# Optimization experiments

Hardware: AMD Instinct MI355X
Metric: run time of the kernel (lower is better)

The kernel has to match this reference:

```python
import jax, jax.numpy as jnp
import numpy as np

T, G = 8, 128                      # time frames, spatial grid per axis
RMIN, RMAX = -1.5, 1.5             # same range for x, y, z
STEP = (RMAX - RMIN) / G           # voxel step per axis
# corner order: [C000, C100, C010, C110, C001, C101, C011, C111]
_OFFSETS = jnp.array([[0,0,0],[1,0,0],[0,1,0],[1,1,0],
                      [0,0,1],[1,0,1],[0,1,1],[1,1,1]], dtype=jnp.int32)

def _trilinear_coef(p):
    # p: [N,3] fractional position inside the cell, in [0,1)
    u, v, w = p[:, 0], p[:, 1], p[:, 2]
    return jnp.stack([(1-u)*(1-v)*(1-w), u*(1-v)*(1-w), (1-u)*v*(1-w), u*v*(1-w),
                      (1-u)*(1-v)*w,     u*(1-v)*w,     (1-u)*v*w,     u*v*w], axis=1)

def setup_inputs() -> dict:
    key = jax.random.key(0)
    k1, k2, k3, k4 = jax.random.split(key, 4)
    N = 1048576
    pos = jax.random.uniform(k1, (N, 3), jnp.float32, RMIN, RMAX)
    t = jax.random.randint(k2, (N,), 0, T, dtype=jnp.int32)
    sigma = jax.random.uniform(k3, (N,), jnp.float32)
    target_norm = jax.random.normal(k4, (N, 3), jnp.float32)
    lr = jnp.full((1,), 0.1, jnp.float32)
    voxel_array = jnp.full((T, G, G, G, 3), jnp.sqrt(1.0 / 3.0), jnp.float32)
    return {"t": t, "pos": pos, "lr": lr, "sigma": sigma,
            "target_norm": target_norm, "voxel_array": voxel_array}

def reference(t, pos, lr, sigma, target_norm, voxel_array):
    # shift into [0, range) coords (all axes share the same range/step)
    pos_s = pos - RMIN
    min_idx = jnp.floor(pos_s / STEP).astype(jnp.int32)          # [N,3], == // in source
    idx = jnp.clip(min_idx[:, None, :] + _OFFSETS[None], 0, G - 1)  # [N,8,3]
    frac = jnp.mod(pos_s, STEP) / STEP                           # [N,3]
    coef = _trilinear_coef(frac)                                 # [N,8]
    xi, yi, zi = idx[..., 0], idx[..., 1], idx[..., 2]
    ti = jnp.broadcast_to(t[:, None], xi.shape)                  # [N,8]
    vertex_values = voxel_array[ti, xi, yi, zi]                  # [N,8,3] gather
    value = jnp.sum(coef[:, :, None] * vertex_values, axis=1)    # [N,3]
    # update weights
    sigma_weight = (1.0 - jnp.exp(-sigma))[:, None]              # [N,1]
    update_lambda = jax.nn.sigmoid(lr * sigma_weight * coef)[..., None]  # [N,8,1]
    new_vertex_values = update_lambda * target_norm[:, None, :] + (1.0 - update_lambda) * vertex_values
    diff = new_vertex_values - vertex_values                     # [N,8,3]
    new_voxel = voxel_array.at[ti.reshape(-1), xi.reshape(-1),
                               yi.reshape(-1), zi.reshape(-1)].add(diff.reshape(-1, 3))
    return value, new_voxel
```

## Files before the change

kernel.cpp:

```cpp
#include <hip/hip_runtime.h>
#include <hip/hip_fp16.h>
#include <math.h>


#define GRES 128
#define NBINS (8 * 128 * 128)
#define SCAN_BLOCKS 512
constexpr float RMIN_F = -1.5f;
constexpr float STEP_F = 3.0f / 128.0f;

__global__ __launch_bounds__(256) void key_hist_kernel(
    const int* __restrict__ t, const float* __restrict__ pos,
    unsigned* __restrict__ keys, unsigned* __restrict__ hist, int N)
{
    int i = blockIdx.x * blockDim.x + threadIdx.x;
    if (i >= N) return;
    float px = pos[3 * i + 0] - RMIN_F;
    float py = pos[3 * i + 1] - RMIN_F;
    int cx = min((int)floorf(px / STEP_F), GRES - 1);
    int cy = min((int)floorf(py / STEP_F), GRES - 1);
    unsigned key  = ((unsigned)t[i] << 14) | ((unsigned)cx << 7) | (unsigned)cy;
    unsigned rank = atomicAdd(&hist[key], 1u);
    keys[i] = (key << 15) | rank;
}

__global__ __launch_bounds__(256) void scanA_kernel(
    const unsigned* __restrict__ hist, unsigned* __restrict__ binstart,
    unsigned* __restrict__ partial)
{
    __shared__ unsigned sh[256];
    const int tid = threadIdx.x;
    const int gid = blockIdx.x * 256 + tid;
    unsigned x = hist[gid];
    sh[tid] = x;
    __syncthreads();
    for (int off = 1; off < 256; off <<= 1) {
        unsigned v = (tid >= off) ? sh[tid - off] : 0u;
        __syncthreads();
        sh[tid] += v;
        __syncthreads();
    }
    binstart[gid] = sh[tid] - x;
    if (tid == 255) partial[blockIdx.x] = sh[255];
}

__global__ __launch_bounds__(512) void scanB_kernel(
    const unsigned* __restrict__ partial, unsigned* __restrict__ offs)
{
    __shared__ unsigned sh[512];
    const int tid = threadIdx.x;
    unsigned x = partial[tid];
    sh[tid] = x;
    __syncthreads();
    for (int off = 1; off < 512; off <<= 1) {
        unsigned v = (tid >= off) ? sh[tid - off] : 0u;
        __syncthreads();
        sh[tid] += v;
        __syncthreads();
    }
    offs[tid] = sh[tid] - x;
}

__global__ __launch_bounds__(256) void scanC_kernel(
    unsigned* __restrict__ binstart, const unsigned* __restrict__ offs, int N)
{
    const int gid = blockIdx.x * 256 + threadIdx.x;
    binstart[gid] += offs[blockIdx.x];
    if (gid == 0) binstart[NBINS] = (unsigned)N;
}

__global__ __launch_bounds__(256) void scatter_kernel(
    const float* __restrict__ pos, const float* __restrict__ lr_p,
    const float* __restrict__ sigma, const float* __restrict__ target,
    const unsigned* __restrict__ keys, const unsigned* __restrict__ binstart,
    uint4* __restrict__ sorted, int N)
{
    int i = blockIdx.x * blockDim.x + threadIdx.x;
    if (i >= N) return;
    unsigned kr   = keys[i];
    unsigned key  = kr >> 15;
    unsigned rank = kr & 0x7fffu;
    unsigned slot = binstart[key] + rank;

    float px = pos[3 * i + 0] - RMIN_F;
    float py = pos[3 * i + 1] - RMIN_F;
    float pz = pos[3 * i + 2] - RMIN_F;
    float u = fmodf(px, STEP_F) / STEP_F;
    float v = fmodf(py, STEP_F) / STEP_F;
    float w = fmodf(pz, STEP_F) / STEP_F;
    int   mz = min((int)floorf(pz / STEP_F), GRES - 1);

    unsigned qu = (unsigned)(u * 2047.0f + 0.5f);
    unsigned qv = (unsigned)(v * 2047.0f + 0.5f);
    unsigned qw = (unsigned)(w * 1023.0f + 0.5f);

    float lrsw = lr_p[0] * (1.0f - expf(-sigma[i]));

    unsigned hx = (unsigned)__half_as_ushort(__float2half(target[3 * i + 0]));
    unsigned hy = (unsigned)__half_as_ushort(__float2half(target[3 * i + 1]));
    unsigned hz = (unsigned)__half_as_ushort(__float2half(target[3 * i + 2]));
    unsigned hl = (unsigned)__half_as_ushort(__float2half(lrsw));

    uint4 p;
    p.x = (qu << 21) | (qv << 10) | qw;
    p.y = ((unsigned)i << 7) | (unsigned)mz;
    p.z = hx | (hy << 16);
    p.w = hz | (hl << 16);
    sorted[slot] = p;
}

__global__ __launch_bounds__(256) void brick_kernel(
    const unsigned* __restrict__ binstart,
    const uint4*    __restrict__ sorted,
    const float*    __restrict__ voxel_in,
    float*          __restrict__ out_value,
    float*          __restrict__ out_voxel)
{
    __shared__ __align__(16) float s_acc[4 * 4 * 128 * 3];
    __shared__ unsigned s_start[25];
    __shared__ unsigned s_pref[26];

    const int vb = ((blockIdx.x & 7) << 10) | (blockIdx.x >> 3);
    const int t  = vb >> 10;
    const int bx = (vb >> 5) & 31;
    const int by = vb & 31;
    const int x0 = bx << 2, y0 = by << 2;
    const int tid = threadIdx.x;
    const size_t tbase = (size_t)t * (GRES * GRES * GRES * 3);

    float4* s_acc4 = (float4*)s_acc;
    for (int q = tid; q < 16 * 96; q += 256) s_acc4[q] = make_float4(0.f, 0.f, 0.f, 0.f);

    if (tid < 25) {
        int dxb = tid / 5 - 1, dyb = tid % 5 - 1;
        int cx = x0 + dxb, cy = y0 + dyb;
        unsigned st = 0, cnt = 0;
        if (cx >= 0 && cx < GRES && cy >= 0 && cy < GRES) {
            unsigned key = ((unsigned)t << 14) | ((unsigned)cx << 7) | (unsigned)cy;
            st  = binstart[key];
            cnt = binstart[key + 1] - st;
        }
        s_start[tid] = st;
        s_pref[tid + 1] = cnt;
    }
    __syncthreads();
    if (tid == 0) {
        unsigned run = 0;
        s_pref[0] = 0;
        for (int b = 0; b < 25; ++b) {
            unsigned c = s_pref[b + 1];
            s_pref[b + 1] = run + c;
            run += c;
        }
    }
    __syncthreads();
    const int P = (int)s_pref[25];

    for (int j = tid; j < P; j += 256) {
        int b = 0;
        while (s_pref[b + 1] <= (unsigned)j) ++b;
        const int dxb = b / 5 - 1, dyb = b % 5 - 1;
        const int cx = x0 + dxb, cy = y0 + dyb;
        const unsigned g = s_start[b] + ((unsigned)j - s_pref[b]);

        const uint4 p = sorted[g];
        const float u = (float)(p.x >> 21)           * (1.0f / 2047.0f);
        const float v = (float)((p.x >> 10) & 2047u) * (1.0f / 2047.0f);
        const float w = (float)(p.x & 1023u)         * (1.0f / 1023.0f);
        const int  mz  = (int)(p.y & 127u);
        const int  idx = (int)(p.y >> 7);
        const float tx = __half2float(__ushort_as_half((unsigned short)(p.z & 0xffffu)));
        const float ty = __half2float(__ushort_as_half((unsigned short)(p.z >> 16)));
        const float tz = __half2float(__ushort_as_half((unsigned short)(p.w & 0xffffu)));
        const float lrsw = __half2float(__ushort_as_half((unsigned short)(p.w >> 16)));

        const int xs1 = min(cx + 1, GRES - 1);
        const int ys1 = min(cy + 1, GRES - 1);
        const int zs1 = min(mz + 1, GRES - 1);

        float a[8][3];
        #pragma unroll
        for (int k = 0; k < 8; ++k) {
            const int xi = (k & 1) ? xs1 : cx;
            const int yi = (k & 2) ? ys1 : cy;
            const int zi = (k & 4) ? zs1 : mz;
            const float* vp = voxel_in + tbase + (((size_t)xi * GRES + yi) * GRES + zi) * 3;
            a[k][0] = vp[0];
            a[k][1] = vp[1];
            a[k][2] = vp[2];
        }

        float c[8];
        c[0] = (1.f - u) * (1.f - v) * (1.f - w);
        c[1] =        u  * (1.f - v) * (1.f - w);
        c[2] = (1.f - u) *        v  * (1.f - w);
        c[3] =        u  *        v  * (1.f - w);
        c[4] = (1.f - u) * (1.f - v) *        w;
        c[5] =        u  * (1.f - v) *        w;
        c[6] = (1.f - u) *        v  *        w;
        c[7] =        u  *        v  *        w;

        const bool owner = (dxb >= 0) && (dyb >= 0);

        float vx = 0.f, vy = 0.f, vz = 0.f;
        #pragma unroll
        for (int k = 0; k < 8; ++k) {
            if (owner) {
                vx += c[k] * a[k][0];
                vy += c[k] * a[k][1];
                vz += c[k] * a[k][2];
            }
            const int xi = (k & 1) ? xs1 : cx;
            const int yi = (k & 2) ? ys1 : cy;
            const int sxi = xi - x0, syi = yi - y0;
            if (sxi >= 0 && sxi < 4 && syi >= 0 && syi < 4) {
                const int zi = (k & 4) ? zs1 : mz;
                const float lam = 1.0f / (1.0f + expf(-lrsw * c[k]));
                const int sa = ((sxi * 4 + syi) * 128 + zi) * 3;
                atomicAdd(&s_acc[sa + 0], lam * (tx - a[k][0]));
                atomicAdd(&s_acc[sa + 1], lam * (ty - a[k][1]));
                atomicAdd(&s_acc[sa + 2], lam * (tz - a[k][2]));
            }
        }
        if (owner) {
            out_value[3 * idx + 0] = vx;
            out_value[3 * idx + 1] = vy;
            out_value[3 * idx + 2] = vz;
        }
    }
    __syncthreads();

    for (int q = tid; q < 16 * 96; q += 256) {
        int row = q / 96, r = q - row * 96;
        int ox = row >> 2, oy = row & 3;
        const size_t coff = tbase + (size_t)(x0 + ox) * 49152 + (size_t)(y0 + oy) * 384;
        float4 a = *((const float4*)(voxel_in + coff) + r);
        float4 d = s_acc4[q];
        *((float4*)(out_voxel + coff) + r) =
            make_float4(a.x + d.x, a.y + d.y, a.z + d.z, a.w + d.w);
    }
}

extern "C" void kernel_launch(void* const* d_in, const int* in_sizes, int n_in,
                              void* d_out, int out_size, void* d_ws, size_t ws_size,
                              hipStream_t stream) {
    const int*   t      = (const int*)  d_in[0];
    const float* pos    = (const float*)d_in[1];
    const float* lr     = (const float*)d_in[2];
    const float* sigma  = (const float*)d_in[3];
    const float* target = (const float*)d_in[4];
    const float* voxel  = (const float*)d_in[5];

    const int N = in_sizes[0];

    float* out_value = (float*)d_out;
    float* out_voxel = out_value + (size_t)3 * N;

    uint4*    sorted   = (uint4*)d_ws;
    unsigned* keys     = (unsigned*)(sorted + (size_t)N);
    unsigned* hist     = keys + N;
    unsigned* binstart = hist + NBINS;
    unsigned* partial  = binstart + (NBINS + 1);
    unsigned* offs     = partial + SCAN_BLOCKS;

    const int block = 256;
    const int grid  = (N + block - 1) / block;

    hipMemsetAsync(hist, 0, NBINS * sizeof(unsigned), stream);
    key_hist_kernel<<<grid, block, 0, stream>>>(t, pos, keys, hist, N);
    scanA_kernel<<<SCAN_BLOCKS, 256, 0, stream>>>(hist, binstart, partial);
    scanB_kernel<<<1, 512, 0, stream>>>(partial, offs);
    scanC_kernel<<<SCAN_BLOCKS, 256, 0, stream>>>(binstart, offs, N);
    scatter_kernel<<<grid, block, 0, stream>>>(pos, lr, sigma, target, keys,
                                               binstart, sorted, N);
    brick_kernel<<<8192, 256, 0, stream>>>(binstart, sorted, voxel,
                                           out_value, out_voxel);
}
```

Measured before the change: 523.7 us.

## Accumulate lambda-weighted sums in shared memory, gather corners only for owners, merge scan

The brick kernel now accumulates sum(lam), sum(lam*target) per voxel in float4 shared slots. The old value is applied once at write-out, so per-particle corner gathers of the voxel array are needed only for owner particles that produce the interpolated value. This rests on the update being linear in the old voxel value. The scanB kernel is removed, and each scanC block reduces its preceding partials itself. The change also uses fast __expf and binary search for the bin lookup. Shared memory grows (float4 per voxel, 4 atomics instead of 3), and the final write-out loses float4 vectorisation in exchange for fewer global gathers.

```diff
diff --git a/kernel.cpp b/kernel.cpp
--- a/kernel.cpp
+++ b/kernel.cpp
@@ -44,28 +44,19 @@
     if (tid == 255) partial[blockIdx.x] = sh[255];
 }
 
-__global__ __launch_bounds__(512) void scanB_kernel(
-    const unsigned* __restrict__ partial, unsigned* __restrict__ offs)
-{
-    __shared__ unsigned sh[512];
-    const int tid = threadIdx.x;
-    unsigned x = partial[tid];
-    sh[tid] = x;
-    __syncthreads();
-    for (int off = 1; off < 512; off <<= 1) {
-        unsigned v = (tid >= off) ? sh[tid - off] : 0u;
-        __syncthreads();
-        sh[tid] += v;
-        __syncthreads();
-    }
-    offs[tid] = sh[tid] - x;
-}
-
 __global__ __launch_bounds__(256) void scanC_kernel(
-    unsigned* __restrict__ binstart, const unsigned* __restrict__ offs, int N)
-{
+    unsigned* __restrict__ binstart, const unsigned* __restrict__ partial, int N)
+{
+    __shared__ unsigned s_w[4];
+    unsigned loc = 0;
+    for (int i = threadIdx.x; i < blockIdx.x; i += 256) loc += partial[i];
+    #pragma unroll
+    for (int off = 32; off > 0; off >>= 1) loc += __shfl_down(loc, off);
+    if ((threadIdx.x & 63) == 0) s_w[threadIdx.x >> 6] = loc;
+    __syncthreads();
+    const unsigned off0 = s_w[0] + s_w[1] + s_w[2] + s_w[3];
     const int gid = blockIdx.x * 256 + threadIdx.x;
-    binstart[gid] += offs[blockIdx.x];
+    binstart[gid] += off0;
     if (gid == 0) binstart[NBINS] = (unsigned)N;
 }
 
@@ -94,7 +85,7 @@
     unsigned qv = (unsigned)(v * 2047.0f + 0.5f);
     unsigned qw = (unsigned)(w * 1023.0f + 0.5f);
 
-    float lrsw = lr_p[0] * (1.0f - expf(-sigma[i]));
+    float lrsw = lr_p[0] * (1.0f - __expf(-sigma[i]));
 
     unsigned hx = (unsigned)__half_as_ushort(__float2half(target[3 * i + 0]));
     unsigned hy = (unsigned)__half_as_ushort(__float2half(target[3 * i + 1]));
@@ -116,7 +107,7 @@
     float*          __restrict__ out_value,
     float*          __restrict__ out_voxel)
 {
-    __shared__ __align__(16) float s_acc[4 * 4 * 128 * 3];
+    __shared__ __align__(16) float4 s_acc[4 * 4 * 128];
     __shared__ unsigned s_start[25];
     __shared__ unsigned s_pref[26];
 
@@ -128,8 +119,7 @@
     const int tid = threadIdx.x;
     const size_t tbase = (size_t)t * (GRES * GRES * GRES * 3);
 
-    float4* s_acc4 = (float4*)s_acc;
-    for (int q = tid; q < 16 * 96; q += 256) s_acc4[q] = make_float4(0.f, 0.f, 0.f, 0.f);
+    for (int q = tid; q < 2048; q += 256) s_acc[q] = make_float4(0.f, 0.f, 0.f, 0.f);
 
     if (tid < 25) {
         int dxb = tid / 5 - 1, dyb = tid % 5 - 1;
@@ -148,9 +138,8 @@
         unsigned run = 0;
         s_pref[0] = 0;
         for (int b = 0; b < 25; ++b) {
-            unsigned c = s_pref[b + 1];
-            s_pref[b + 1] = run + c;
-            run += c;
+            run += s_pref[b + 1];
+            s_pref[b + 1] = run;
         }
     }
     __syncthreads();
@@ -158,7 +147,11 @@
 
     for (int j = tid; j < P; j += 256) {
         int b = 0;
-        while (s_pref[b + 1] <= (unsigned)j) ++b;
+        #pragma unroll
+        for (int s = 16; s > 0; s >>= 1) {
+            int nb = b + s;
+            if (nb <= 24 && s_pref[nb] <= (unsigned)j) b = nb;
+        }
         const int dxb = b / 5 - 1, dyb = b % 5 - 1;
         const int cx = x0 + dxb, cy = y0 + dyb;
         const unsigned g = s_start[b] + ((unsigned)j - s_pref[b]);
@@ -178,18 +171,6 @@
         const int ys1 = min(cy + 1, GRES - 1);
         const int zs1 = min(mz + 1, GRES - 1);
 
-        float a[8][3];
-        #pragma unroll
-        for (int k = 0; k < 8; ++k) {
-            const int xi = (k & 1) ? xs1 : cx;
-            const int yi = (k & 2) ? ys1 : cy;
-            const int zi = (k & 4) ? zs1 : mz;
-            const float* vp = voxel_in + tbase + (((size_t)xi * GRES + yi) * GRES + zi) * 3;
-            a[k][0] = vp[0];
-            a[k][1] = vp[1];
-            a[k][2] = vp[2];
-        }
-
         float c[8];
         c[0] = (1.f - u) * (1.f - v) * (1.f - w);
         c[1] =        u  * (1.f - v) * (1.f - w);
@@ -202,42 +183,61 @@
 
         const bool owner = (dxb >= 0) && (dyb >= 0);
 
-        float vx = 0.f, vy = 0.f, vz = 0.f;
-        #pragma unroll
-        for (int k = 0; k < 8; ++k) {
-            if (owner) {
+        if (owner) {
+            float a[8][3];
+            #pragma unroll
+            for (int k = 0; k < 8; ++k) {
+                const int xi = (k & 1) ? xs1 : cx;
+                const int yi = (k & 2) ? ys1 : cy;
+                const int zi = (k & 4) ? zs1 : mz;
+                const float* vp = voxel_in + tbase + (((size_t)xi * GRES + yi) * GRES + zi) * 3;
+                a[k][0] = vp[0];
+                a[k][1] = vp[1];
+                a[k][2] = vp[2];
+            }
+            float vx = 0.f, vy = 0.f, vz = 0.f;
+            #pragma unroll
+            for (int k = 0; k < 8; ++k) {
                 vx += c[k] * a[k][0];
                 vy += c[k] * a[k][1];
                 vz += c[k] * a[k][2];
             }
+            out_value[3 * idx + 0] = vx;
+            out_value[3 * idx + 1] = vy;
+            out_value[3 * idx + 2] = vz;
+        }
+
+        #pragma unroll
+        for (int k = 0; k < 8; ++k) {
             const int xi = (k & 1) ? xs1 : cx;
             const int yi = (k & 2) ? ys1 : cy;
             const int sxi = xi - x0, syi = yi - y0;
             if (sxi >= 0 && sxi < 4 && syi >= 0 && syi < 4) {
                 const int zi = (k & 4) ? zs1 : mz;
-                const float lam = 1.0f / (1.0f + expf(-lrsw * c[k]));
-                const int sa = ((sxi * 4 + syi) * 128 + zi) * 3;
-                atomicAdd(&s_acc[sa + 0], lam * (tx - a[k][0]));
-                atomicAdd(&s_acc[sa + 1], lam * (ty - a[k][1]));
-                atomicAdd(&s_acc[sa + 2], lam * (tz - a[k][2]));
+                const float lam = 1.0f / (1.0f + __expf(-lrsw * c[k]));
+                float* sa = (float*)&s_acc[(sxi * 4 + syi) * 128 + zi];
+                atomicAdd(sa + 0, lam);
+                atomicAdd(sa + 1, lam * tx);
+                atomicAdd(sa + 2, lam * ty);
+                atomicAdd(sa + 3, lam * tz);
             }
         }
-        if (owner) {
-            out_value[3 * idx + 0] = vx;
-            out_value[3 * idx + 1] = vy;
-            out_value[3 * idx + 2] = vz;
-        }
-    }
-    __syncthreads();
-
-    for (int q = tid; q < 16 * 96; q += 256) {
-        int row = q / 96, r = q - row * 96;
-        int ox = row >> 2, oy = row & 3;
-        const size_t coff = tbase + (size_t)(x0 + ox) * 49152 + (size_t)(y0 + oy) * 384;
-        float4 a = *((const float4*)(voxel_in + coff) + r);
-        float4 d = s_acc4[q];
-        *((float4*)(out_voxel + coff) + r) =
-            make_float4(a.x + d.x, a.y + d.y, a.z + d.z, a.w + d.w);
+    }
+    __syncthreads();
+
+    for (int q = tid; q < 2048; q += 256) {
+        const int col = q >> 7;
+        const int zi  = q & 127;
+        const int ox = col >> 2, oy = col & 3;
+        const size_t coff = tbase + (size_t)(x0 + ox) * 49152
+                                  + (size_t)(y0 + oy) * 384 + 3 * (size_t)zi;
+        const float4 s = s_acc[q];
+        const float ax = voxel_in[coff + 0];
+        const float ay = voxel_in[coff + 1];
+        const float az = voxel_in[coff + 2];
+        out_voxel[coff + 0] = ax + s.y - s.x * ax;
+        out_voxel[coff + 1] = ay + s.z - s.x * ay;
+        out_voxel[coff + 2] = az + s.w - s.x * az;
     }
 }
 
@@ -261,7 +261,6 @@
     unsigned* hist     = keys + N;
     unsigned* binstart = hist + NBINS;
     unsigned* partial  = binstart + (NBINS + 1);
-    unsigned* offs     = partial + SCAN_BLOCKS;
 
     const int block = 256;
     const int grid  = (N + block - 1) / block;
@@ -269,8 +268,7 @@
     hipMemsetAsync(hist, 0, NBINS * sizeof(unsigned), stream);
     key_hist_kernel<<<grid, block, 0, stream>>>(t, pos, keys, hist, N);
     scanA_kernel<<<SCAN_BLOCKS, 256, 0, stream>>>(hist, binstart, partial);
-    scanB_kernel<<<1, 512, 0, stream>>>(partial, offs);
-    scanC_kernel<<<SCAN_BLOCKS, 256, 0, stream>>>(binstart, offs, N);
+    scanC_kernel<<<SCAN_BLOCKS, 256, 0, stream>>>(binstart, partial, N);
     scatter_kernel<<<grid, block, 0, stream>>>(pos, lr, sigma, target, keys,
                                                binstart, sorted, N);
     brick_kernel<<<8192, 256, 0, stream>>>(binstart, sorted, voxel,
```

Result: slower. 580.1 us (+10.8%).

## Fuse binning pipeline into one cooperative kernel and widen brick blocks

Applied to the files above, without the earlier changes.

Merges the memset, histogram, three-stage scan and scatter into a single cooperative kernel with grid-wide syncs, so the separate launches and inter-kernel gaps go away. The brick kernel moves to 512 threads per block, computes its 25-bin prefix with a wavefront shuffle scan, and finds each particle's bin by binary search instead of a linear scan. It also switches expf to the faster __expf intrinsic. Costs: the grid syncs force a fixed grid of 1024 blocks that must all be co-resident, and the larger brick blocks may lower occupancy.

```diff
diff --git a/kernel.cpp b/kernel.cpp
--- a/kernel.cpp
+++ b/kernel.cpp
@@ -1,115 +1,113 @@
 #include <hip/hip_runtime.h>
 #include <hip/hip_fp16.h>
+#include <hip/hip_cooperative_groups.h>
 #include <math.h>
+
+namespace cg = cooperative_groups;
 
 
 #define GRES 128
 #define NBINS (8 * 128 * 128)
-#define SCAN_BLOCKS 512
+#define SCAN_VBLOCKS 512
+#define PRESORT_BLOCKS 1024
 constexpr float RMIN_F = -1.5f;
 constexpr float STEP_F = 3.0f / 128.0f;
 
-__global__ __launch_bounds__(256) void key_hist_kernel(
-    const int* __restrict__ t, const float* __restrict__ pos,
-    unsigned* __restrict__ keys, unsigned* __restrict__ hist, int N)
+__global__ __launch_bounds__(256, 4) void presort_kernel(
+    const int*   __restrict__ t,     const float* __restrict__ pos,
+    const float* __restrict__ lr_p,  const float* __restrict__ sigma,
+    const float* __restrict__ target,
+    unsigned* __restrict__ keys,     unsigned* __restrict__ hist,
+    unsigned* __restrict__ binstart, unsigned* __restrict__ partial,
+    uint4*    __restrict__ sorted,   int N)
 {
-    int i = blockIdx.x * blockDim.x + threadIdx.x;
-    if (i >= N) return;
-    float px = pos[3 * i + 0] - RMIN_F;
-    float py = pos[3 * i + 1] - RMIN_F;
-    int cx = min((int)floorf(px / STEP_F), GRES - 1);
-    int cy = min((int)floorf(py / STEP_F), GRES - 1);
-    unsigned key  = ((unsigned)t[i] << 14) | ((unsigned)cx << 7) | (unsigned)cy;
-    unsigned rank = atomicAdd(&hist[key], 1u);
-    keys[i] = (key << 15) | rank;
+    cg::grid_group grid = cg::this_grid();
+    const int tid  = threadIdx.x;
+    const int gtid = blockIdx.x * 256 + tid;
+    const int gsz  = PRESORT_BLOCKS * 256;
+
+    for (int i = gtid; i < NBINS; i += gsz) hist[i] = 0u;
+    grid.sync();
+
+    for (int i = gtid; i < N; i += gsz) {
+        float px = pos[3 * i + 0] - RMIN_F;
+        float py = pos[3 * i + 1] - RMIN_F;
+        int cx = min((int)floorf(px / STEP_F), GRES - 1);
+        int cy = min((int)floorf(py / STEP_F), GRES - 1);
+        unsigned key  = ((unsigned)t[i] << 14) | ((unsigned)cx << 7) | (unsigned)cy;
+        unsigned rank = atomicAdd(&hist[key], 1u);
+        keys[i] = (key << 15) | rank;
+    }
+    grid.sync();
+
+    __shared__ unsigned sh[256];
+    if (blockIdx.x < SCAN_VBLOCKS) {
+        const int gid = blockIdx.x * 256 + tid;
+        unsigned x = hist[gid];
+        sh[tid] = x;
+        __syncthreads();
+        for (int off = 1; off < 256; off <<= 1) {
+            unsigned v = (tid >= off) ? sh[tid - off] : 0u;
+            __syncthreads();
+            sh[tid] += v;
+            __syncthreads();
+        }
+        binstart[gid] = sh[tid] - x;
+        if (tid == 255) partial[blockIdx.x] = sh[255];
+    }
+    grid.sync();
+
+    if (blockIdx.x < SCAN_VBLOCKS) {
+        __shared__ unsigned s_w[4];
+        unsigned loc = 0;
+        for (int i = tid; i < blockIdx.x; i += 256) loc += partial[i];
+        #pragma unroll
+        for (int off = 32; off > 0; off >>= 1) loc += __shfl_down(loc, off);
+        if ((tid & 63) == 0) s_w[tid >> 6] = loc;
+        __syncthreads();
+        const unsigned off0 = s_w[0] + s_w[1] + s_w[2] + s_w[3];
+        const int gid = blockIdx.x * 256 + tid;
+        binstart[gid] += off0;
+        if (gid == 0) binstart[NBINS] = (unsigned)N;
+    }
+    grid.sync();
+
+    const float lr0 = lr_p[0];
+    for (int i = gtid; i < N; i += gsz) {
+        unsigned kr   = keys[i];
+        unsigned key  = kr >> 15;
+        unsigned rank = kr & 0x7fffu;
+        unsigned slot = binstart[key] + rank;
+
+        float px = pos[3 * i + 0] - RMIN_F;
+        float py = pos[3 * i + 1] - RMIN_F;
+        float pz = pos[3 * i + 2] - RMIN_F;
+        float u = fmodf(px, STEP_F) / STEP_F;
+        float v = fmodf(py, STEP_F) / STEP_F;
+        float w = fmodf(pz, STEP_F) / STEP_F;
+        int   mz = min((int)floorf(pz / STEP_F), GRES - 1);
+
+        unsigned qu = (unsigned)(u * 2047.0f + 0.5f);
+        unsigned qv = (unsigned)(v * 2047.0f + 0.5f);
+        unsigned qw = (unsigned)(w * 1023.0f + 0.5f);
+
+        float lrsw = lr0 * (1.0f - __expf(-sigma[i]));
+
+        unsigned hx = (unsigned)__half_as_ushort(__float2half(target[3 * i + 0]));
+        unsigned hy = (unsigned)__half_as_ushort(__float2half(target[3 * i + 1]));
+        unsigned hz = (unsigned)__half_as_ushort(__float2half(target[3 * i + 2]));
+        unsigned hl = (unsigned)__half_as_ushort(__float2half(lrsw));
+
+        uint4 p;
+        p.x = (qu << 21) | (qv << 10) | qw;
+        p.y = ((unsigned)i << 7) | (unsigned)mz;
+        p.z = hx | (hy << 16);
+        p.w = hz | (hl << 16);
+        sorted[slot] = p;
+    }
 }
 
-__global__ __launch_bounds__(256) void scanA_kernel(
-    const unsigned* __restrict__ hist, unsigned* __restrict__ binstart,
-    unsigned* __restrict__ partial)
-{
-    __shared__ unsigned sh[256];
-    const int tid = threadIdx.x;
-    const int gid = blockIdx.x * 256 + tid;
-    unsigned x = hist[gid];
-    sh[tid] = x;
-    __syncthreads();
-    for (int off = 1; off < 256; off <<= 1) {
-        unsigned v = (tid >= off) ? sh[tid - off] : 0u;
-        __syncthreads();
-        sh[tid] += v;
-        __syncthreads();
-    }
-    binstart[gid] = sh[tid] - x;
-    if (tid == 255) partial[blockIdx.x] = sh[255];
-}
-
-__global__ __launch_bounds__(512) void scanB_kernel(
-    const unsigned* __restrict__ partial, unsigned* __restrict__ offs)
-{
-    __shared__ unsigned sh[512];
-    const int tid = threadIdx.x;
-    unsigned x = partial[tid];
-    sh[tid] = x;
-    __syncthreads();
-    for (int off = 1; off < 512; off <<= 1) {
-        unsigned v = (tid >= off) ? sh[tid - off] : 0u;
-        __syncthreads();
-        sh[tid] += v;
-        __syncthreads();
-    }
-    offs[tid] = sh[tid] - x;
-}
-
-__global__ __launch_bounds__(256) void scanC_kernel(
-    unsigned* __restrict__ binstart, const unsigned* __restrict__ offs, int N)
-{
-    const int gid = blockIdx.x * 256 + threadIdx.x;
-    binstart[gid] += offs[blockIdx.x];
-    if (gid == 0) binstart[NBINS] = (unsigned)N;
-}
-
-__global__ __launch_bounds__(256) void scatter_kernel(
-    const float* __restrict__ pos, const float* __restrict__ lr_p,
-    const float* __restrict__ sigma, const float* __restrict__ target,
-    const unsigned* __restrict__ keys, const unsigned* __restrict__ binstart,
-    uint4* __restrict__ sorted, int N)
-{
-    int i = blockIdx.x * blockDim.x + threadIdx.x;
-    if (i >= N) return;
-    unsigned kr   = keys[i];
-    unsigned key  = kr >> 15;
-    unsigned rank = kr & 0x7fffu;
-    unsigned slot = binstart[key] + rank;
-
-    float px = pos[3 * i + 0] - RMIN_F;
-    float py = pos[3 * i + 1] - RMIN_F;
-    float pz = pos[3 * i + 2] - RMIN_F;
-    float u = fmodf(px, STEP_F) / STEP_F;
-    float v = fmodf(py, STEP_F) / STEP_F;
-    float w = fmodf(pz, STEP_F) / STEP_F;
-    int   mz = min((int)floorf(pz / STEP_F), GRES - 1);
-
-    unsigned qu = (unsigned)(u * 2047.0f + 0.5f);
-    unsigned qv = (unsigned)(v * 2047.0f + 0.5f);
-    unsigned qw = (unsigned)(w * 1023.0f + 0.5f);
-
-    float lrsw = lr_p[0] * (1.0f - expf(-sigma[i]));
-
-    unsigned hx = (unsigned)__half_as_ushort(__float2half(target[3 * i + 0]));
-    unsigned hy = (unsigned)__half_as_ushort(__float2half(target[3 * i + 1]));
-    unsigned hz = (unsigned)__half_as_ushort(__float2half(target[3 * i + 2]));
-    unsigned hl = (unsigned)__half_as_ushort(__float2half(lrsw));
-
-    uint4 p;
-    p.x = (qu << 21) | (qv << 10) | qw;
-    p.y = ((unsigned)i << 7) | (unsigned)mz;
-    p.z = hx | (hy << 16);
-    p.w = hz | (hl << 16);
-    sorted[slot] = p;
-}
-
-__global__ __launch_bounds__(256) void brick_kernel(
+__global__ __launch_bounds__(512, 8) void brick_kernel(
     const unsigned* __restrict__ binstart,
     const uint4*    __restrict__ sorted,
     const float*    __restrict__ voxel_in,
@@ -129,36 +127,39 @@
     const size_t tbase = (size_t)t * (GRES * GRES * GRES * 3);
 
     float4* s_acc4 = (float4*)s_acc;
-    for (int q = tid; q < 16 * 96; q += 256) s_acc4[q] = make_float4(0.f, 0.f, 0.f, 0.f);
-
-    if (tid < 25) {
-        int dxb = tid / 5 - 1, dyb = tid % 5 - 1;
-        int cx = x0 + dxb, cy = y0 + dyb;
+    for (int q = tid; q < 16 * 96; q += 512) s_acc4[q] = make_float4(0.f, 0.f, 0.f, 0.f);
+
+    if (tid < 64) {
         unsigned st = 0, cnt = 0;
-        if (cx >= 0 && cx < GRES && cy >= 0 && cy < GRES) {
-            unsigned key = ((unsigned)t << 14) | ((unsigned)cx << 7) | (unsigned)cy;
-            st  = binstart[key];
-            cnt = binstart[key + 1] - st;
-        }
-        s_start[tid] = st;
-        s_pref[tid + 1] = cnt;
-    }
-    __syncthreads();
-    if (tid == 0) {
-        unsigned run = 0;
-        s_pref[0] = 0;
-        for (int b = 0; b < 25; ++b) {
-            unsigned c = s_pref[b + 1];
-            s_pref[b + 1] = run + c;
-            run += c;
-        }
+        if (tid < 25) {
+            int dxb = tid / 5 - 1, dyb = tid % 5 - 1;
+            int cx = x0 + dxb, cy = y0 + dyb;
+            if (cx >= 0 && cx < GRES && cy >= 0 && cy < GRES) {
+                unsigned key = ((unsigned)t << 14) | ((unsigned)cx << 7) | (unsigned)cy;
+                st  = binstart[key];
+                cnt = binstart[key + 1] - st;
+            }
+            s_start[tid] = st;
+        }
+        unsigned x = cnt;
+        #pragma unroll
+        for (int off = 1; off < 32; off <<= 1) {
+            unsigned y = __shfl_up(x, off);
+            if (tid >= off) x += y;
+        }
+        if (tid < 25) s_pref[tid + 1] = x;
+        if (tid == 0) s_pref[0] = 0;
     }
     __syncthreads();
     const int P = (int)s_pref[25];
 
-    for (int j = tid; j < P; j += 256) {
+    for (int j = tid; j < P; j += 512) {
         int b = 0;
-        while (s_pref[b + 1] <= (unsigned)j) ++b;
+        #pragma unroll
+        for (int s = 16; s > 0; s >>= 1) {
+            int nb = b + s;
+            if (nb <= 24 && s_pref[nb] <= (unsigned)j) b = nb;
+        }
         const int dxb = b / 5 - 1, dyb = b % 5 - 1;
         const int cx = x0 + dxb, cy = y0 + dyb;
         const unsigned g = s_start[b] + ((unsigned)j - s_pref[b]);
@@ -215,7 +216,7 @@
             const int sxi = xi - x0, syi = yi - y0;
             if (sxi >= 0 && sxi < 4 && syi >= 0 && syi < 4) {
                 const int zi = (k & 4) ? zs1 : mz;
-                const float lam = 1.0f / (1.0f + expf(-lrsw * c[k]));
+                const float lam = 1.0f / (1.0f + __expf(-lrsw * c[k]));
                 const int sa = ((sxi * 4 + syi) * 128 + zi) * 3;
                 atomicAdd(&s_acc[sa + 0], lam * (tx - a[k][0]));
                 atomicAdd(&s_acc[sa + 1], lam * (ty - a[k][1]));
@@ -230,7 +231,7 @@
     }
     __syncthreads();
 
-    for (int q = tid; q < 16 * 96; q += 256) {
+    for (int q = tid; q < 16 * 96; q += 512) {
         int row = q / 96, r = q - row * 96;
         int ox = row >> 2, oy = row & 3;
         const size_t coff = tbase + (size_t)(x0 + ox) * 49152 + (size_t)(y0 + oy) * 384;
@@ -261,18 +262,15 @@
     unsigned* hist     = keys + N;
     unsigned* binstart = hist + NBINS;
     unsigned* partial  = binstart + (NBINS + 1);
-    unsigned* offs     = partial + SCAN_BLOCKS;
-
-    const int block = 256;
-    const int grid  = (N + block - 1) / block;
-
-    hipMemsetAsync(hist, 0, NBINS * sizeof(unsigned), stream);
-    key_hist_kernel<<<grid, block, 0, stream>>>(t, pos, keys, hist, N);
-    scanA_kernel<<<SCAN_BLOCKS, 256, 0, stream>>>(hist, binstart, partial);
-    scanB_kernel<<<1, 512, 0, stream>>>(partial, offs);
-    scanC_kernel<<<SCAN_BLOCKS, 256, 0, stream>>>(binstart, offs, N);
-    scatter_kernel<<<grid, block, 0, stream>>>(pos, lr, sigma, target, keys,
-                                               binstart, sorted, N);
-    brick_kernel<<<8192, 256, 0, stream>>>(binstart, sorted, voxel,
+
+    int n = N;
+    void* args[] = { (void*)&t, (void*)&pos, (void*)&lr, (void*)&sigma,
+                     (void*)&target, (void*)&keys, (void*)&hist,
+                     (void*)&binstart, (void*)&partial, (void*)&sorted,
+                     (void*)&n };
+    hipLaunchCooperativeKernel((const void*)presort_kernel,
+                               dim3(PRESORT_BLOCKS), dim3(256),
+                               args, 0, stream);
+    brick_kernel<<<8192, 512, 0, stream>>>(binstart, sorted, voxel,
                                            out_value, out_voxel);
 }
```

New measurement: 895.4 us. 71.0% more time.

## Replace counting sort with fixed-capacity bins plus overflow list

Applied to the files above, without the earlier changes.

Particles are now placed directly into fixed-capacity (16) per-(t,x,y) bins in one pass, with an overflow list for bins that fill up. This replaces the histogram, scan and scatter passes, so only two kernels run. The brick kernel reads the capped bins and then scans the overflow list for events belonging to its neighbourhood. The change also switches to fast __expf, a wave-shuffle prefix sum and a binary search for bin lookup. It costs a large workspace (NBINS*16*16 bytes), adds sparse bin reads, and events beyond OVF_MAX would be silently dropped. The old path stays as a fallback when the workspace is too small.

```diff
diff --git a/kernel.cpp b/kernel.cpp
--- a/kernel.cpp
+++ b/kernel.cpp
@@ -5,9 +5,61 @@
 
 #define GRES 128
 #define NBINS (8 * 128 * 128)
+#define CAP 16
+#define OVF_MAX 16384
 #define SCAN_BLOCKS 512
 constexpr float RMIN_F = -1.5f;
 constexpr float STEP_F = 3.0f / 128.0f;
+
+__device__ __forceinline__ uint4 make_payload(
+    int i, float px, float py, float pz, int mz,
+    const float* __restrict__ target, float lrsw)
+{
+    float u = fmodf(px, STEP_F) / STEP_F;
+    float v = fmodf(py, STEP_F) / STEP_F;
+    float w = fmodf(pz, STEP_F) / STEP_F;
+    unsigned qu = (unsigned)(u * 2047.0f + 0.5f);
+    unsigned qv = (unsigned)(v * 2047.0f + 0.5f);
+    unsigned qw = (unsigned)(w * 1023.0f + 0.5f);
+    unsigned hx = (unsigned)__half_as_ushort(__float2half(target[3 * i + 0]));
+    unsigned hy = (unsigned)__half_as_ushort(__float2half(target[3 * i + 1]));
+    unsigned hz = (unsigned)__half_as_ushort(__float2half(target[3 * i + 2]));
+    unsigned hl = (unsigned)__half_as_ushort(__float2half(lrsw));
+    uint4 p;
+    p.x = (qu << 21) | (qv << 10) | qw;
+    p.y = ((unsigned)i << 7) | (unsigned)mz;
+    p.z = hx | (hy << 16);
+    p.w = hz | (hl << 16);
+    return p;
+}
+
+__global__ __launch_bounds__(256) void place_kernel(
+    const int*   __restrict__ t,     const float* __restrict__ pos,
+    const float* __restrict__ lr_p,  const float* __restrict__ sigma,
+    const float* __restrict__ target,
+    unsigned* __restrict__ hist,     uint4* __restrict__ bins,
+    unsigned* __restrict__ ovfcnt,   unsigned* __restrict__ ovf_key,
+    uint4*    __restrict__ ovf_pay,  int N)
+{
+    int i = blockIdx.x * blockDim.x + threadIdx.x;
+    if (i >= N) return;
+    float px = pos[3 * i + 0] - RMIN_F;
+    float py = pos[3 * i + 1] - RMIN_F;
+    float pz = pos[3 * i + 2] - RMIN_F;
+    int cx = min((int)floorf(px / STEP_F), GRES - 1);
+    int cy = min((int)floorf(py / STEP_F), GRES - 1);
+    int mz = min((int)floorf(pz / STEP_F), GRES - 1);
+    float lrsw = lr_p[0] * (1.0f - __expf(-sigma[i]));
+    uint4 p = make_payload(i, px, py, pz, mz, target, lrsw);
+    unsigned key  = ((unsigned)t[i] << 14) | ((unsigned)cx << 7) | (unsigned)cy;
+    unsigned rank = atomicAdd(&hist[key], 1u);
+    if (rank < CAP) {
+        bins[(size_t)key * CAP + rank] = p;
+    } else {
+        unsigned o = atomicAdd(ovfcnt, 1u);
+        if (o < OVF_MAX) { ovf_key[o] = key; ovf_pay[o] = p; }
+    }
+}
 
 __global__ __launch_bounds__(256) void key_hist_kernel(
     const int* __restrict__ t, const float* __restrict__ pos,
@@ -44,28 +96,19 @@
     if (tid == 255) partial[blockIdx.x] = sh[255];
 }
 
-__global__ __launch_bounds__(512) void scanB_kernel(
-    const unsigned* __restrict__ partial, unsigned* __restrict__ offs)
-{
-    __shared__ unsigned sh[512];
-    const int tid = threadIdx.x;
-    unsigned x = partial[tid];
-    sh[tid] = x;
+__global__ __launch_bounds__(256) void scanC_kernel(
+    unsigned* __restrict__ binstart, const unsigned* __restrict__ partial, int N)
+{
+    __shared__ unsigned s_w[4];
+    unsigned loc = 0;
+    for (int i = threadIdx.x; i < blockIdx.x; i += 256) loc += partial[i];
+    #pragma unroll
+    for (int off = 32; off > 0; off >>= 1) loc += __shfl_down(loc, off);
+    if ((threadIdx.x & 63) == 0) s_w[threadIdx.x >> 6] = loc;
     __syncthreads();
-    for (int off = 1; off < 512; off <<= 1) {
-        unsigned v = (tid >= off) ? sh[tid - off] : 0u;
-        __syncthreads();
-        sh[tid] += v;
-        __syncthreads();
-    }
-    offs[tid] = sh[tid] - x;
-}
-
-__global__ __launch_bounds__(256) void scanC_kernel(
-    unsigned* __restrict__ binstart, const unsigned* __restrict__ offs, int N)
-{
+    const unsigned off0 = s_w[0] + s_w[1] + s_w[2] + s_w[3];
     const int gid = blockIdx.x * 256 + threadIdx.x;
-    binstart[gid] += offs[blockIdx.x];
+    binstart[gid] += off0;
     if (gid == 0) binstart[NBINS] = (unsigned)N;
 }
 
@@ -81,44 +124,100 @@
     unsigned key  = kr >> 15;
     unsigned rank = kr & 0x7fffu;
     unsigned slot = binstart[key] + rank;
-
     float px = pos[3 * i + 0] - RMIN_F;
     float py = pos[3 * i + 1] - RMIN_F;
     float pz = pos[3 * i + 2] - RMIN_F;
-    float u = fmodf(px, STEP_F) / STEP_F;
-    float v = fmodf(py, STEP_F) / STEP_F;
-    float w = fmodf(pz, STEP_F) / STEP_F;
     int   mz = min((int)floorf(pz / STEP_F), GRES - 1);
-
-    unsigned qu = (unsigned)(u * 2047.0f + 0.5f);
-    unsigned qv = (unsigned)(v * 2047.0f + 0.5f);
-    unsigned qw = (unsigned)(w * 1023.0f + 0.5f);
-
-    float lrsw = lr_p[0] * (1.0f - expf(-sigma[i]));
-
-    unsigned hx = (unsigned)__half_as_ushort(__float2half(target[3 * i + 0]));
-    unsigned hy = (unsigned)__half_as_ushort(__float2half(target[3 * i + 1]));
-    unsigned hz = (unsigned)__half_as_ushort(__float2half(target[3 * i + 2]));
-    unsigned hl = (unsigned)__half_as_ushort(__float2half(lrsw));
-
-    uint4 p;
-    p.x = (qu << 21) | (qv << 10) | qw;
-    p.y = ((unsigned)i << 7) | (unsigned)mz;
-    p.z = hx | (hy << 16);
-    p.w = hz | (hl << 16);
-    sorted[slot] = p;
+    float lrsw = lr_p[0] * (1.0f - __expf(-sigma[i]));
+    sorted[slot] = make_payload(i, px, py, pz, mz, target, lrsw);
+}
+
+__device__ __forceinline__ void process_event(
+    const uint4 p, const int cx, const int cy,
+    const int x0, const int y0, const size_t tbase,
+    const float* __restrict__ voxel_in,
+    float* __restrict__ out_value, float* __restrict__ s_acc)
+{
+    const float u = (float)(p.x >> 21)           * (1.0f / 2047.0f);
+    const float v = (float)((p.x >> 10) & 2047u) * (1.0f / 2047.0f);
+    const float w = (float)(p.x & 1023u)         * (1.0f / 1023.0f);
+    const int  mz  = (int)(p.y & 127u);
+    const int  idx = (int)(p.y >> 7);
+    const float tx = __half2float(__ushort_as_half((unsigned short)(p.z & 0xffffu)));
+    const float ty = __half2float(__ushort_as_half((unsigned short)(p.z >> 16)));
+    const float tz = __half2float(__ushort_as_half((unsigned short)(p.w & 0xffffu)));
+    const float lrsw = __half2float(__ushort_as_half((unsigned short)(p.w >> 16)));
+
+    const int xs1 = min(cx + 1, GRES - 1);
+    const int ys1 = min(cy + 1, GRES - 1);
+    const int zs1 = min(mz + 1, GRES - 1);
+
+    float a[8][3];
+    #pragma unroll
+    for (int k = 0; k < 8; ++k) {
+        const int xi = (k & 1) ? xs1 : cx;
+        const int yi = (k & 2) ? ys1 : cy;
+        const int zi = (k & 4) ? zs1 : mz;
+        const float* vp = voxel_in + tbase + (((size_t)xi * GRES + yi) * GRES + zi) * 3;
+        a[k][0] = vp[0];
+        a[k][1] = vp[1];
+        a[k][2] = vp[2];
+    }
+
+    float c[8];
+    c[0] = (1.f - u) * (1.f - v) * (1.f - w);
+    c[1] =        u  * (1.f - v) * (1.f - w);
+    c[2] = (1.f - u) *        v  * (1.f - w);
+    c[3] =        u  *        v  * (1.f - w);
+    c[4] = (1.f - u) * (1.f - v) *        w;
+    c[5] =        u  * (1.f - v) *        w;
+    c[6] = (1.f - u) *        v  *        w;
+    c[7] =        u  *        v  *        w;
+
+    const bool owner = (cx >= x0) && (cy >= y0);
+
+    float vx = 0.f, vy = 0.f, vz = 0.f;
+    #pragma unroll
+    for (int k = 0; k < 8; ++k) {
+        if (owner) {
+            vx += c[k] * a[k][0];
+            vy += c[k] * a[k][1];
+            vz += c[k] * a[k][2];
+        }
+        const int xi = (k & 1) ? xs1 : cx;
+        const int yi = (k & 2) ? ys1 : cy;
+        const int sxi = xi - x0, syi = yi - y0;
+        if (sxi >= 0 && sxi < 4 && syi >= 0 && syi < 4) {
+            const int zi = (k & 4) ? zs1 : mz;
+            const float lam = 1.0f / (1.0f + __expf(-lrsw * c[k]));
+            const int sa = ((sxi * 4 + syi) * 128 + zi) * 3;
+            atomicAdd(&s_acc[sa + 0], lam * (tx - a[k][0]));
+            atomicAdd(&s_acc[sa + 1], lam * (ty - a[k][1]));
+            atomicAdd(&s_acc[sa + 2], lam * (tz - a[k][2]));
+        }
+    }
+    if (owner) {
+        out_value[3 * idx + 0] = vx;
+        out_value[3 * idx + 1] = vy;
+        out_value[3 * idx + 2] = vz;
+    }
 }
 
 __global__ __launch_bounds__(256) void brick_kernel(
-    const unsigned* __restrict__ binstart,
+    const unsigned* __restrict__ counts,
     const uint4*    __restrict__ sorted,
     const float*    __restrict__ voxel_in,
     float*          __restrict__ out_value,
-    float*          __restrict__ out_voxel)
+    float*          __restrict__ out_voxel,
+    int cap,
+    const unsigned* __restrict__ ovf_key,
+    const uint4*    __restrict__ ovf_pay,
+    const unsigned* __restrict__ ovfcnt)
 {
     __shared__ __align__(16) float s_acc[4 * 4 * 128 * 3];
     __shared__ unsigned s_start[25];
     __shared__ unsigned s_pref[26];
+    __shared__ unsigned s_novf;
 
     const int vb = ((blockIdx.x & 7) << 10) | (blockIdx.x >> 3);
     const int t  = vb >> 10;
@@ -131,101 +230,57 @@
     float4* s_acc4 = (float4*)s_acc;
     for (int q = tid; q < 16 * 96; q += 256) s_acc4[q] = make_float4(0.f, 0.f, 0.f, 0.f);
 
-    if (tid < 25) {
-        int dxb = tid / 5 - 1, dyb = tid % 5 - 1;
-        int cx = x0 + dxb, cy = y0 + dyb;
+    if (tid < 64) {
         unsigned st = 0, cnt = 0;
-        if (cx >= 0 && cx < GRES && cy >= 0 && cy < GRES) {
-            unsigned key = ((unsigned)t << 14) | ((unsigned)cx << 7) | (unsigned)cy;
-            st  = binstart[key];
-            cnt = binstart[key + 1] - st;
-        }
-        s_start[tid] = st;
-        s_pref[tid + 1] = cnt;
-    }
-    __syncthreads();
-    if (tid == 0) {
-        unsigned run = 0;
-        s_pref[0] = 0;
-        for (int b = 0; b < 25; ++b) {
-            unsigned c = s_pref[b + 1];
-            s_pref[b + 1] = run + c;
-            run += c;
-        }
-    }
+        if (tid < 25) {
+            int dxb = tid / 5 - 1, dyb = tid % 5 - 1;
+            int cx = x0 + dxb, cy = y0 + dyb;
+            if (cx >= 0 && cx < GRES && cy >= 0 && cy < GRES) {
+                unsigned key = ((unsigned)t << 14) | ((unsigned)cx << 7) | (unsigned)cy;
+                if (cap > 0) {
+                    st  = key * (unsigned)cap;
+                    cnt = min(counts[key], (unsigned)cap);
+                } else {
+                    st  = counts[key];
+                    cnt = counts[key + 1] - st;
+                }
+            }
+            s_start[tid] = st;
+        }
+        unsigned x = cnt;
+        #pragma unroll
+        for (int off = 1; off < 32; off <<= 1) {
+            unsigned y = __shfl_up(x, off);
+            if (tid >= off) x += y;
+        }
+        if (tid < 25) s_pref[tid + 1] = x;
+        if (tid == 0) s_pref[0] = 0;
+    }
+    if (tid == 64) s_novf = (cap > 0) ? *ovfcnt : 0u;
     __syncthreads();
     const int P = (int)s_pref[25];
 
     for (int j = tid; j < P; j += 256) {
         int b = 0;
-        while (s_pref[b + 1] <= (unsigned)j) ++b;
-        const int dxb = b / 5 - 1, dyb = b % 5 - 1;
-        const int cx = x0 + dxb, cy = y0 + dyb;
+        #pragma unroll
+        for (int s = 16; s > 0; s >>= 1) {
+            int nb = b + s;
+            if (nb <= 24 && s_pref[nb] <= (unsigned)j) b = nb;
+        }
+        const int cx = x0 + b / 5 - 1, cy = y0 + b % 5 - 1;
         const unsigned g = s_start[b] + ((unsigned)j - s_pref[b]);
-
-        const uint4 p = sorted[g];
-        const float u = (float)(p.x >> 21)           * (1.0f / 2047.0f);
-        const float v = (float)((p.x >> 10) & 2047u) * (1.0f / 2047.0f);
-        const float w = (float)(p.x & 1023u)         * (1.0f / 1023.0f);
-        const int  mz  = (int)(p.y & 127u);
-        const int  idx = (int)(p.y >> 7);
-        const float tx = __half2float(__ushort_as_half((unsigned short)(p.z & 0xffffu)));
-        const float ty = __half2float(__ushort_as_half((unsigned short)(p.z >> 16)));
-        const float tz = __half2float(__ushort_as_half((unsigned short)(p.w & 0xffffu)));
-        const float lrsw = __half2float(__ushort_as_half((unsigned short)(p.w >> 16)));
-
-        const int xs1 = min(cx + 1, GRES - 1);
-        const int ys1 = min(cy + 1, GRES - 1);
-        const int zs1 = min(mz + 1, GRES - 1);
-
-        float a[8][3];
-        #pragma unroll
-        for (int k = 0; k < 8; ++k) {
-            const int xi = (k & 1) ? xs1 : cx;
-            const int yi = (k & 2) ? ys1 : cy;
-            const int zi = (k & 4) ? zs1 : mz;
-            const float* vp = voxel_in + tbase + (((size_t)xi * GRES + yi) * GRES + zi) * 3;
-            a[k][0] = vp[0];
-            a[k][1] = vp[1];
-            a[k][2] = vp[2];
-        }
-
-        float c[8];
-        c[0] = (1.f - u) * (1.f - v) * (1.f - w);
-        c[1] =        u  * (1.f - v) * (1.f - w);
-        c[2] = (1.f - u) *        v  * (1.f - w);
-        c[3] =        u  *        v  * (1.f - w);
-        c[4] = (1.f - u) * (1.f - v) *        w;
-        c[5] =        u  * (1.f - v) *        w;
-        c[6] = (1.f - u) *        v  *        w;
-        c[7] =        u  *        v  *        w;
-
-        const bool owner = (dxb >= 0) && (dyb >= 0);
-
-        float vx = 0.f, vy = 0.f, vz = 0.f;
-        #pragma unroll
-        for (int k = 0; k < 8; ++k) {
-            if (owner) {
-                vx += c[k] * a[k][0];
-                vy += c[k] * a[k][1];
-                vz += c[k] * a[k][2];
-            }
-            const int xi = (k & 1) ? xs1 : cx;
-            const int yi = (k & 2) ? ys1 : cy;
-            const int sxi = xi - x0, syi = yi - y0;
-            if (sxi >= 0 && sxi < 4 && syi >= 0 && syi < 4) {
-                const int zi = (k & 4) ? zs1 : mz;
-                const float lam = 1.0f / (1.0f + expf(-lrsw * c[k]));
-                const int sa = ((sxi * 4 + syi) * 128 + zi) * 3;
-                atomicAdd(&s_acc[sa + 0], lam * (tx - a[k][0]));
-                atomicAdd(&s_acc[sa + 1], lam * (ty - a[k][1]));
-                atomicAdd(&s_acc[sa + 2], lam * (tz - a[k][2]));
-            }
-        }
-        if (owner) {
-            out_value[3 * idx + 0] = vx;
-            out_value[3 * idx + 1] = vy;
-            out_value[3 * idx + 2] = vz;
+        process_event(sorted[g], cx, cy, x0, y0, tbase, voxel_in, out_value, s_acc);
+    }
+
+    if (cap > 0) {
+        const unsigned novf = min(s_novf, (unsigned)OVF_MAX);
+        for (unsigned o = tid; o < novf; o += 256) {
+            const unsigned key = ovf_key[o];
+            if ((int)(key >> 14) != t) continue;
+            const int ocx = (int)((key >> 7) & 127u), ocy = (int)(key & 127u);
+            const int dxb = ocx - x0, dyb = ocy - y0;
+            if (dxb < -1 || dxb > 3 || dyb < -1 || dyb > 3) continue;
+            process_event(ovf_pay[o], ocx, ocy, x0, y0, tbase, voxel_in, out_value, s_acc);
         }
     }
     __syncthreads();
@@ -256,23 +311,41 @@
     float* out_value = (float*)d_out;
     float* out_voxel = out_value + (size_t)3 * N;
 
-    uint4*    sorted   = (uint4*)d_ws;
-    unsigned* keys     = (unsigned*)(sorted + (size_t)N);
-    unsigned* hist     = keys + N;
-    unsigned* binstart = hist + NBINS;
-    unsigned* partial  = binstart + (NBINS + 1);
-    unsigned* offs     = partial + SCAN_BLOCKS;
-
     const int block = 256;
     const int grid  = (N + block - 1) / block;
 
-    hipMemsetAsync(hist, 0, NBINS * sizeof(unsigned), stream);
-    key_hist_kernel<<<grid, block, 0, stream>>>(t, pos, keys, hist, N);
-    scanA_kernel<<<SCAN_BLOCKS, 256, 0, stream>>>(hist, binstart, partial);
-    scanB_kernel<<<1, 512, 0, stream>>>(partial, offs);
-    scanC_kernel<<<SCAN_BLOCKS, 256, 0, stream>>>(binstart, offs, N);
-    scatter_kernel<<<grid, block, 0, stream>>>(pos, lr, sigma, target, keys,
-                                               binstart, sorted, N);
-    brick_kernel<<<8192, 256, 0, stream>>>(binstart, sorted, voxel,
-                                           out_value, out_voxel);
-}
+    const size_t need = (size_t)NBINS * CAP * 16 + (size_t)NBINS * 4 + 64
+                      + (size_t)OVF_MAX * 4 + (size_t)OVF_MAX * 16;
+
+    if (ws_size >= need) {
+        uint4*    bins    = (uint4*)d_ws;
+        unsigned* hist    = (unsigned*)(bins + (size_t)NBINS * CAP);
+        unsigned* ovfcnt  = hist + NBINS;
+        unsigned* ovf_key = ovfcnt + 16;
+        uint4*    ovf_pay = (uint4*)(ovf_key + OVF_MAX);
+
+        hipMemsetAsync(hist, 0, NBINS * sizeof(unsigned) + 64, stream);
+        place_kernel<<<grid, block, 0, stream>>>(t, pos, lr, sigma, target,
+                                                 hist, bins, ovfcnt, ovf_key,
+                                                 ovf_pay, N);
+        brick_kernel<<<8192, 256, 0, stream>>>(hist, bins, voxel,
+                                               out_value, out_voxel,
+                                               CAP, ovf_key, ovf_pay, ovfcnt);
+    } else {
+        uint4*    sorted   = (uint4*)d_ws;
+        unsigned* keys     = (unsigned*)(sorted + (size_t)N);
+        unsigned* hist     = keys + N;
+        unsigned* binstart = hist + NBINS;
+        unsigned* partial  = binstart + (NBINS + 1);
+
+        hipMemsetAsync(hist, 0, NBINS * sizeof(unsigned), stream);
+        key_hist_kernel<<<grid, block, 0, stream>>>(t, pos, keys, hist, N);
+        scanA_kernel<<<SCAN_BLOCKS, 256, 0, stream>>>(hist, binstart, partial);
+        scanC_kernel<<<SCAN_BLOCKS, 256, 0, stream>>>(binstart, partial, N);
+        scatter_kernel<<<grid, block, 0, stream>>>(pos, lr, sigma, target, keys,
+                                                   binstart, sorted, N);
+        brick_kernel<<<8192, 256, 0, stream>>>(binstart, sorted, voxel,
+                                               out_value, out_voxel,
+                                               0, nullptr, nullptr, nullptr);
+    }
+}
```

New measurement: 515.1 us. No clear change (-1.6%).
